# Performance work log

Hardware: AMD Instinct MI355X
Metric: run time of the kernel (lower is better)

The kernel has to match this reference:

```python
import jax, jax.numpy as jnp
import numpy as np

H_SZ, W_SZ = 24, 24  # size for location=2 (H*W == N3)

def _ln(x, g, b, eps=1e-5):
    m = jnp.mean(x, axis=-1, keepdims=True)
    v = jnp.var(x, axis=-1, keepdims=True)
    return (x - m) / jnp.sqrt(v + eps) * g + b

def _cross_attn(value, x2, Wp, bp):
    # key = softmax(x2^T, dim=1) == softmax over channels; query = softmax over tokens
    k = jax.nn.softmax(x2, axis=2)   # [B,M,C], softmax over C
    q = jax.nn.softmax(x2, axis=1)   # [B,M,C], softmax over M
    ctx = jnp.einsum('bnc,bmc->bnm', value, k)   # value @ key
    att = jnp.einsum('bnm,bmc->bnc', ctx, q)     # context @ query
    return att @ Wp.T + bp

def _dwconv(x, Wdw, bdw, Hh, Ww):
    B, N, C = x.shape
    t = x.transpose(0, 2, 1).reshape(B, C, Hh, Ww)
    y = jax.lax.conv_general_dilated(t, Wdw, (1, 1), 'SAME',
                                     feature_group_count=C,
                                     dimension_numbers=('NCHW', 'OIHW', 'NCHW'))
    y = y + bdw[None, :, None, None]
    return y.reshape(B, C, N).transpose(0, 2, 1)

def setup_inputs() -> dict:
    key = jax.random.key(0)
    ks = jax.random.split(key, 16)
    B = 4; d0, d1, d2 = 128, 256, 512
    N1, N2, N3 = 96 * 96, 48 * 48, 24 * 24
    s = 0.02
    dh = 4 * d2
    inp = {}
    inp['x']  = jax.random.normal(ks[0], (B, N1, d0), jnp.float32)
    inp['x2'] = jax.random.normal(ks[1], (B, N2, d1), jnp.float32)
    inp['x3'] = jax.random.normal(ks[2], (B, N3, d2), jnp.float32)
    inp['W_lin']  = jax.random.normal(ks[3], (d2, d0)) * s   # linear: d0->d2
    inp['W_lin2'] = jax.random.normal(ks[4], (d2, d1)) * s   # linear2: d1->d2
    inp['W_lin3'] = jax.random.normal(ks[5], (d1, d0)) * s   # linear3: d0->d1
    inp['W_lin4'] = jax.random.normal(ks[6], (d2, d1)) * s   # linear4: d1->d2
    inp['w'] = jnp.ones((1,), jnp.float32)
    inp['Wp1'] = jax.random.normal(ks[7], (d2, d2)) * s;  inp['bp1'] = jnp.zeros((d2,))
    inp['Wp2'] = jax.random.normal(ks[8], (d2, d2)) * s;  inp['bp2'] = jnp.zeros((d2,))
    inp['Wp3'] = jax.random.normal(ks[9], (d1, d1)) * s;  inp['bp3'] = jnp.zeros((d1,))
    inp['Wp4'] = jax.random.normal(ks[10], (d2, d2)) * s; inp['bp4'] = jnp.zeros((d2,))
    inp['g_norm'] = jnp.ones((d2,)); inp['b_norm'] = jnp.zeros((d2,))
    inp['Wfc1'] = jax.random.normal(ks[11], (dh, d2)) * s; inp['bfc1'] = jnp.zeros((dh,))
    inp['Wdw']  = jax.random.normal(ks[12], (dh, 1, 3, 3)) * s; inp['bdw'] = jnp.zeros((dh,))
    inp['g_ln1'] = jnp.ones((dh,)); inp['b_ln1'] = jnp.zeros((dh,))
    inp['Wfc2'] = jax.random.normal(ks[13], (d2, dh)) * s; inp['bfc2'] = jnp.zeros((d2,))
    return inp

def reference(x, x2, x3, W_lin, W_lin2, W_lin3, W_lin4, w,
              Wp1, bp1, Wp2, bp2, Wp3, bp3, Wp4, bp4,
              g_norm, b_norm, Wfc1, bfc1, Wdw, bdw, g_ln1, b_ln1, Wfc2, bfc2):
    # location == 2 branch
    image  = x  @ W_lin.T    # [B,N1,d2]
    image2 = x2 @ W_lin2.T   # [B,N2,d2]
    image4 = x  @ W_lin3.T   # [B,N1,d1]
    atten1 = _cross_attn(x3, image,  Wp1, bp1)
    atten2 = _cross_attn(x3, image2, Wp2, bp2)
    a3 = _cross_attn(x2, image4, Wp3, bp3)   # [B,N2,d1]
    a3 = a3 @ W_lin4.T                        # [B,N2,d2]
    atten3 = _cross_attn(x3, a3, Wp4, bp4)    # [B,N3,d2]
    f = jax.nn.sigmoid(w)
    other = (1.0 - f) / 2.0
    atten_ = f * atten3 + other * atten2 + other * atten1
    atten = x3 + atten_
    an = _ln(atten, g_norm, b_norm)
    # MixFFN_skip (fc1 computed once; torch computes it twice with same result)
    h = an @ Wfc1.T + bfc1
    dw = _dwconv(h, Wdw, bdw, H_SZ, W_SZ)
    ax = jax.nn.gelu(_ln(dw + h, g_ln1, b_ln1), approximate=False)
    out = ax @ Wfc2.T + bfc2
    return atten + out
```

## Files before the change

### kernel.cpp

```cpp
#include <hip/hip_runtime.h>
#include <hip/hip_bf16.h>
#include <math.h>

typedef long long i64;
typedef __attribute__((ext_vector_type(8))) short short8v;
typedef __attribute__((ext_vector_type(4))) float float4v;

#define SPITCH 72
#define NCV 13

__device__ __forceinline__ float ldv(const void* p, i64 idx, int isBf16) {
  return isBf16 ? __bfloat162float(((const __hip_bfloat16*)p)[idx])
                : ((const float*)p)[idx];
}
__device__ __forceinline__ unsigned short bf16bits(float f) {
  __hip_bfloat16 h = __float2bfloat16(f);
  return *(unsigned short*)&h;
}
__device__ __forceinline__ float bits2f(unsigned short u) {
  union { unsigned int ui; float fl; } cv; cv.ui = ((unsigned int)u) << 16;
  return cv.fl;
}

__global__ void detect_dtype(const unsigned short* w, int* dt) {
  dt[0] = (w[0] == 0) ? 0 : 1;
}

struct CvArgs {
  const void* src[NCV];
  unsigned short* dst[NCV];
  i64 n[NCV];
  int blkStart[NCV + 1];
};
__global__ __launch_bounds__(256) void convert_many(const int* dt, CvArgs a) {
  int au = dt[0];
  int bid = blockIdx.x;
  int lo = 0;
  #pragma unroll
  for (int i = 0; i < NCV; ++i) if (bid >= a.blkStart[i + 1]) lo = i + 1;
  const void* s = a.src[lo];
  unsigned short* d = a.dst[lo];
  i64 n = a.n[lo];
  i64 base = ((i64)(bid - a.blkStart[lo]) * 256 + threadIdx.x) * 4;
  if (base + 4 <= n) {
    #pragma unroll
    for (int j = 0; j < 4; ++j) d[base + j] = bf16bits(ldv(s, base + j, au));
  } else {
    for (; base < n; ++base) d[base] = bf16bits(ldv(s, base, au));
  }
}

__global__ void transpose_dw(const int* dt, const void* Wdw, unsigned short* Wdwt) {
  int au = dt[0];
  int i = blockIdx.x * 256 + threadIdx.x;
  if (i >= 9 * 2048) return;
  int k = i / 2048, ch = i % 2048;
  Wdwt[i] = bf16bits(ldv(Wdw, (i64)ch * 9 + k, au));
}

__global__ __launch_bounds__(256) void gemm_mfma_bt(
    const int* dt,
    const unsigned short* A, i64 bsA,
    const unsigned short* Bt, i64 bsB,
    const void* bias, int biasDt,
    const void* add, int addDt, i64 bsAdd,
    void* C, i64 bsC, int outMode,
    int M, int N, int K, int flags,
    const void* wPtr, int alphaMode,
    float* csP, float* rsP)
{
  __shared__ unsigned short Ash[64 * SPITCH];
  __shared__ unsigned short Bsh[64 * SPITCH];
  __shared__ unsigned short LT[64 * SPITCH];

  const int au = dt[0];
  const int bDt = (biasDt == 2) ? au : biasDt;
  const int aDt = (addDt == 2) ? au : addDt;

  const int b  = blockIdx.z;
  const int m0 = blockIdx.y * 64;
  const int n0 = blockIdx.x * 64;
  const int t = threadIdx.x;
  const int lane = t & 63, wave = t >> 6;
  const int wr = (wave >> 1) * 32, wc = (wave & 1) * 32;
  const int quad = lane >> 4, l15 = lane & 15;
  const unsigned short* Ab = A + (i64)b * bsA;
  const unsigned short* Bb = Bt + (i64)b * bsB;
  const int sr = t >> 3, sg = (t & 7) * 8;

  float alpha = 1.0f;
  if (alphaMode) {
    float w0 = ldv(wPtr, 0, au);
    float f = 1.0f / (1.0f + expf(-w0));
    alpha = (alphaMode == 2) ? f : (1.0f - f) * 0.5f;
  }

  float4v acc00 = {0.f,0.f,0.f,0.f}, acc01 = {0.f,0.f,0.f,0.f};
  float4v acc10 = {0.f,0.f,0.f,0.f}, acc11 = {0.f,0.f,0.f,0.f};

  for (int k0 = 0; k0 < K; k0 += 64) {
    #pragma unroll
    for (int p = 0; p < 2; ++p) {
      int rr = sr + p * 32;
      *(short8v*)&Ash[rr * SPITCH + sg] = *(const short8v*)&Ab[(i64)(m0 + rr) * K + k0 + sg];
      *(short8v*)&Bsh[rr * SPITCH + sg] = *(const short8v*)&Bb[(i64)(n0 + rr) * K + k0 + sg];
    }
    __syncthreads();
    #pragma unroll
    for (int ks = 0; ks < 2; ++ks) {
      int ko = ks * 32 + quad * 8;
      short8v a0 = *(const short8v*)&Ash[(wr + l15) * SPITCH + ko];
      short8v a1 = *(const short8v*)&Ash[(wr + 16 + l15) * SPITCH + ko];
      short8v b0 = *(const short8v*)&Bsh[(wc + l15) * SPITCH + ko];
      short8v b1 = *(const short8v*)&Bsh[(wc + 16 + l15) * SPITCH + ko];
      acc00 = __builtin_amdgcn_mfma_f32_16x16x32_bf16(a0, b0, acc00, 0, 0, 0);
      acc01 = __builtin_amdgcn_mfma_f32_16x16x32_bf16(a0, b1, acc01, 0, 0, 0);
      acc10 = __builtin_amdgcn_mfma_f32_16x16x32_bf16(a1, b0, acc10, 0, 0, 0);
      acc11 = __builtin_amdgcn_mfma_f32_16x16x32_bf16(a1, b1, acc11, 0, 0, 0);
    }
    __syncthreads();
  }

  float* Cf = (float*)C;
  unsigned short* Ch = (unsigned short*)C;

  if (outMode == 2) {
    #pragma unroll
    for (int rg = 0; rg < 4; ++rg) {
      #pragma unroll
      for (int sub = 0; sub < 4; ++sub) {
        int lr = wr + quad * 4 + rg + (sub >> 1) * 16;
        int lc = wc + l15 + (sub & 1) * 16;
        float v = (sub == 0 ? acc00[rg] : sub == 1 ? acc01[rg] :
                   sub == 2 ? acc10[rg] : acc11[rg]) * alpha;
        if (bias) v += ldv(bias, n0 + lc, bDt);
        if (flags & 1) v = expf(v);
        LT[lc * SPITCH + lr] = bf16bits(v);
      }
    }
    __syncthreads();
    #pragma unroll
    for (int p = 0; p < 2; ++p) {
      int rr = sr + p * 32;
      short8v vv = *(short8v*)&LT[rr * SPITCH + sg];
      *(short8v*)(Ch + (i64)b * bsC + (i64)(n0 + rr) * M + m0 + sg) = vv;
    }
    if (csP) {
      if (t < 64) {
        const unsigned short* Lr = &LT[t * SPITCH];
        float s = 0.f;
        #pragma unroll
        for (int i = 0; i < 64; ++i) s += bits2f(Lr[i]);
        atomicAdd(&csP[(i64)b * N + n0 + t], s);
      } else if (t < 128) {
        int tok = t - 64;
        float s = 0.f;
        #pragma unroll
        for (int i = 0; i < 64; ++i) s += bits2f(LT[i * SPITCH + tok]);
        atomicAdd(&rsP[(i64)b * M + m0 + tok], s);
      }
    }
    return;
  }

  #pragma unroll
  for (int rg = 0; rg < 4; ++rg) {
    #pragma unroll
    for (int sub = 0; sub < 4; ++sub) {
      int lr = wr + quad * 4 + rg + (sub >> 1) * 16;
      int lc = wc + l15 + (sub & 1) * 16;
      int gi = m0 + lr, gj = n0 + lc;
      float v = (sub == 0 ? acc00[rg] : sub == 1 ? acc01[rg] :
                 sub == 2 ? acc10[rg] : acc11[rg]) * alpha;
      if (bias) v += ldv(bias, gj, bDt);
      if (add)  v += ldv(add, (i64)b * bsAdd + (i64)gi * N + gj, aDt);
      i64 idx = (i64)b * bsC + (i64)gi * N + gj;
      if (flags & 2) v += Cf[idx];
      if (flags & 1) v = expf(v);
      if (outMode == 1) Ch[idx] = bf16bits(v);
      else              Cf[idx] = v;
    }
  }
}

__global__ __launch_bounds__(256) void softprod_sym(
    const unsigned short* Gt, const float* rs, float* Sraw,
    int C, i64 M, int splits, int mChunk)
{
  __shared__ unsigned short At[64 * SPITCH];
  __shared__ unsigned short Bt[64 * SPITCH];
  const int b  = blockIdx.z / splits;
  const int sp = blockIdx.z % splits;
  const int nStrips = C >> 6;
  int rem = blockIdx.x, s0 = 0;
  while (rem >= nStrips - s0) { rem -= nStrips - s0; ++s0; }
  const int s1 = s0 + rem;
  const int c0 = s0 * 64;
  const int c1 = s1 * 64;

  const int t = threadIdx.x;
  const int lane = t & 63, wave = t >> 6;
  const int wr = (wave >> 1) * 32, wc = (wave & 1) * 32;
  const int quad = lane >> 4, l15 = lane & 15;
  const unsigned short* Gb = Gt + (i64)b * C * M;
  const float* rib = rs + (i64)b * M;
  const int sr = t >> 3, sg = (t & 7) * 8;

  float4v acc00 = {0.f,0.f,0.f,0.f}, acc01 = {0.f,0.f,0.f,0.f};
  float4v acc10 = {0.f,0.f,0.f,0.f}, acc11 = {0.f,0.f,0.f,0.f};

  const i64 mBeg = (i64)sp * mChunk, mEnd = mBeg + mChunk;
  for (i64 m0 = mBeg; m0 < mEnd; m0 += 64) {
    float rv[8];
    #pragma unroll
    for (int j = 0; j < 8; ++j) rv[j] = rsqrtf(rib[m0 + sg + j]);
    #pragma unroll
    for (int p = 0; p < 2; ++p) {
      int rr = sr + p * 32;
      short8v va = *(const short8v*)&Gb[(i64)(c0 + rr) * M + m0 + sg];
      short8v vb = *(const short8v*)&Gb[(i64)(c1 + rr) * M + m0 + sg];
      short8v sa, sb;
      #pragma unroll
      for (int j = 0; j < 8; ++j) {
        sa[j] = (short)bf16bits(bits2f((unsigned short)va[j]) * rv[j]);
        sb[j] = (short)bf16bits(bits2f((unsigned short)vb[j]) * rv[j]);
      }
      *(short8v*)&At[rr * SPITCH + sg] = sa;
      *(short8v*)&Bt[rr * SPITCH + sg] = sb;
    }
    __syncthreads();
    #pragma unroll
    for (int ks = 0; ks < 2; ++ks) {
      int ko = ks * 32 + quad * 8;
      short8v a0 = *(const short8v*)&At[(wr + l15) * SPITCH + ko];
      short8v a1 = *(const short8v*)&At[(wr + 16 + l15) * SPITCH + ko];
      short8v b0 = *(const short8v*)&Bt[(wc + l15) * SPITCH + ko];
      short8v b1 = *(const short8v*)&Bt[(wc + 16 + l15) * SPITCH + ko];
      acc00 = __builtin_amdgcn_mfma_f32_16x16x32_bf16(a0, b0, acc00, 0, 0, 0);
      acc01 = __builtin_amdgcn_mfma_f32_16x16x32_bf16(a0, b1, acc01, 0, 0, 0);
      acc10 = __builtin_amdgcn_mfma_f32_16x16x32_bf16(a1, b0, acc10, 0, 0, 0);
      acc11 = __builtin_amdgcn_mfma_f32_16x16x32_bf16(a1, b1, acc11, 0, 0, 0);
    }
    __syncthreads();
  }

  float* Sb = Sraw + (i64)b * C * C;
  #pragma unroll
  for (int rg = 0; rg < 4; ++rg) {
    int r0 = c0 + wr + quad * 4 + rg;
    int cA = c1 + wc + l15;
    atomicAdd(&Sb[(i64)r0 * C + cA],             acc00[rg]);
    atomicAdd(&Sb[(i64)r0 * C + cA + 16],        acc01[rg]);
    atomicAdd(&Sb[(i64)(r0 + 16) * C + cA],      acc10[rg]);
    atomicAdd(&Sb[(i64)(r0 + 16) * C + cA + 16], acc11[rg]);
  }
}

__global__ __launch_bounds__(256) void softprod_sym128(
    const unsigned short* Gt, const float* rs, float* Sraw,
    int C, i64 M, int splits, int mChunk)
{
  __shared__ unsigned short Ash[128 * SPITCH];
  __shared__ unsigned short Bsh[128 * SPITCH];
  const int b  = blockIdx.z / splits;
  const int sp = blockIdx.z % splits;
  const int nStrips = C >> 7;
  int rem = blockIdx.x, s0 = 0;
  while (rem >= nStrips - s0) { rem -= nStrips - s0; ++s0; }
  const int s1 = s0 + rem;
  const int c0 = s0 * 128;
  const int c1 = s1 * 128;

  const int t = threadIdx.x;
  const int lane = t & 63, wave = t >> 6;
  const int wrow = (wave >> 1) * 64, wcol = (wave & 1) * 64;
  const int quad = lane >> 4, l15 = lane & 15;
  const unsigned short* Gb = Gt + (i64)b * C * M;
  const float* rib = rs + (i64)b * M;
  const int sg = (t & 7) * 8;

  float4v acc[4][4];
  #pragma unroll
  for (int i = 0; i < 4; ++i)
    #pragma unroll
    for (int j = 0; j < 4; ++j)
      acc[i][j] = (float4v){0.f, 0.f, 0.f, 0.f};

  const i64 mBeg = (i64)sp * mChunk, mEnd = mBeg + mChunk;
  for (i64 m0 = mBeg; m0 < mEnd; m0 += 64) {
    float rv[8];
    #pragma unroll
    for (int j = 0; j < 8; ++j) rv[j] = rsqrtf(rib[m0 + sg + j]);
    #pragma unroll
    for (int p = 0; p < 4; ++p) {
      int e = t + 256 * p;
      int row = e >> 3;
      short8v va = *(const short8v*)&Gb[(i64)(c0 + row) * M + m0 + sg];
      short8v vb = *(const short8v*)&Gb[(i64)(c1 + row) * M + m0 + sg];
      short8v sa, sb;
      #pragma unroll
      for (int j = 0; j < 8; ++j) {
        sa[j] = (short)bf16bits(bits2f((unsigned short)va[j]) * rv[j]);
        sb[j] = (short)bf16bits(bits2f((unsigned short)vb[j]) * rv[j]);
      }
      *(short8v*)&Ash[row * SPITCH + sg] = sa;
      *(short8v*)&Bsh[row * SPITCH + sg] = sb;
    }
    __syncthreads();
    #pragma unroll
    for (int ks = 0; ks < 2; ++ks) {
      int ko = ks * 32 + quad * 8;
      short8v af[4], bf[4];
      #pragma unroll
      for (int i = 0; i < 4; ++i) {
        af[i] = *(const short8v*)&Ash[(wrow + i * 16 + l15) * SPITCH + ko];
        bf[i] = *(const short8v*)&Bsh[(wcol + i * 16 + l15) * SPITCH + ko];
      }
      #pragma unroll
      for (int i = 0; i < 4; ++i)
        #pragma unroll
        for (int j = 0; j < 4; ++j)
          acc[i][j] = __builtin_amdgcn_mfma_f32_16x16x32_bf16(af[i], bf[j], acc[i][j], 0, 0, 0);
    }
    __syncthreads();
  }

  float* Sb = Sraw + (i64)b * C * C;
  #pragma unroll
  for (int i = 0; i < 4; ++i)
    #pragma unroll
    for (int rg = 0; rg < 4; ++rg) {
      int r = c0 + wrow + i * 16 + quad * 4 + rg;
      #pragma unroll
      for (int j = 0; j < 4; ++j) {
        int cc = c1 + wcol + j * 16 + l15;
        atomicAdd(&Sb[(i64)r * C + cc], acc[i][j][rg]);
      }
    }
}

__global__ void scale_S_sym_bf16(const float* Sraw, const float* cs,
                                 unsigned short* Sb, int C, i64 total) {
  i64 i = (i64)blockIdx.x * blockDim.x + threadIdx.x;
  if (i >= total) return;
  i64 cc2 = (i64)C * C;
  i64 b = i / cc2;
  i64 r = (i % cc2) / C;
  int cp = (int)(i % C);
  const float* Sb_ = Sraw + b * cc2;
  float v = (((int)r >> 6) <= (cp >> 6)) ? Sb_[r * C + cp] : Sb_[(i64)cp * C + r];
  Sb[i] = bf16bits(v / cs[b * C + cp]);
}

__global__ __launch_bounds__(256) void transpose_to_bf16(
    const float* T, unsigned short* Tt, int Nn) {
  __shared__ float tile[64][65];
  int b = blockIdx.z;
  int i0 = blockIdx.y * 64, j0 = blockIdx.x * 64;
  const float* Tb = T + (i64)b * Nn * Nn;
  unsigned short* Ttb = Tt + (i64)b * Nn * Nn;
  int t = threadIdx.x;
  int li = t >> 6, lj = t & 63;
  #pragma unroll
  for (int p = 0; p < 16; ++p)
    tile[li + p * 4][lj] = Tb[(i64)(i0 + li + p * 4) * Nn + j0 + lj];
  __syncthreads();
  #pragma unroll
  for (int p = 0; p < 16; ++p) {
    int row = li + p * 4;
    Ttb[(i64)(j0 + row) * Nn + i0 + lj] = bf16bits(tile[lj][row]);
  }
}

__global__ void combine_bias(const int* dt, const void* w, const void* bp1,
                             const void* bp2, const void* bp4, float* biasc) {
  int au = dt[0];
  int j = threadIdx.x;
  float w0 = ldv(w, 0, au);
  float f = 1.0f / (1.0f + expf(-w0));
  float other = (1.0f - f) * 0.5f;
  biasc[j] = f * ldv(bp4, j, au) + other * (ldv(bp1, j, au) + ldv(bp2, j, au));
}

__global__ __launch_bounds__(256) void layernorm512(const int* dt, const float* X,
                                                    const void* g, const void* be,
                                                    __hip_bfloat16* Y) {
  int au = dt[0];
  i64 row = blockIdx.x;
  const float* xr = X + row * 512;
  int t = threadIdx.x;
  float x0 = xr[t], x1 = xr[t + 256];
  float s = x0 + x1, q = x0 * x0 + x1 * x1;
  #pragma unroll
  for (int off = 32; off; off >>= 1) { s += __shfl_down(s, off); q += __shfl_down(q, off); }
  __shared__ float ws_[4], wq_[4];
  int lane = t & 63, wv = t >> 6;
  if (!lane) { ws_[wv] = s; wq_[wv] = q; }
  __syncthreads();
  float S = ws_[0] + ws_[1] + ws_[2] + ws_[3];
  float Q = wq_[0] + wq_[1] + wq_[2] + wq_[3];
  float mean = S * (1.f / 512.f);
  float var = Q * (1.f / 512.f) - mean * mean;
  float inv = rsqrtf(var + 1e-5f);
  Y[row * 512 + t]       = __float2bfloat16((x0 - mean) * inv * ldv(g, t, au) + ldv(be, t, au));
  Y[row * 512 + t + 256] = __float2bfloat16((x1 - mean) * inv * ldv(g, t + 256, au) + ldv(be, t + 256, au));
}

__global__ __launch_bounds__(256) void dwconv_ln_gelu(
    const int* dt,
    const unsigned short* h, const unsigned short* Wdwt, const void* bdw,
    const void* g, const void* be, unsigned short* ax)
{
  int au = dt[0];
  int n = blockIdx.x;
  int b = blockIdx.y;
  int y = n / 24, x = n % 24;
  const unsigned short* hb = h + (i64)b * 576 * 2048;
  int t = threadIdx.x;
  int ch0 = t * 8;

  float accv[8];
  #pragma unroll
  for (int j = 0; j < 8; ++j) accv[j] = ldv(bdw, ch0 + j, au);

  #pragma unroll
  for (int dy = 0; dy < 3; ++dy) {
    int yy = y + dy - 1;
    if (yy < 0 || yy >= 24) continue;
    #pragma unroll
    for (int dx = 0; dx < 3; ++dx) {
      int xx = x + dx - 1;
      if (xx < 0 || xx >= 24) continue;
      short8v hv = *(const short8v*)&hb[(i64)(yy * 24 + xx) * 2048 + ch0];
      short8v wv = *(const short8v*)&Wdwt[(i64)(dy * 3 + dx) * 2048 + ch0];
      #pragma unroll
      for (int j = 0; j < 8; ++j)
        accv[j] += bits2f((unsigned short)hv[j]) * bits2f((unsigned short)wv[j]);
    }
  }

  short8v hc = *(const short8v*)&hb[(i64)n * 2048 + ch0];
  float z[8];
  float s = 0.f, q = 0.f;
  #pragma unroll
  for (int j = 0; j < 8; ++j) {
    float zz = accv[j] + bits2f((unsigned short)hc[j]);
    z[j] = zz; s += zz; q += zz * zz;
  }

  #pragma unroll
  for (int off = 32; off; off >>= 1) { s += __shfl_down(s, off); q += __shfl_down(q, off); }
  __shared__ float ws_[4], wq_[4];
  int lane = t & 63, wv2 = t >> 6;
  if (!lane) { ws_[wv2] = s; wq_[wv2] = q; }
  __syncthreads();
  float S = ws_[0] + ws_[1] + ws_[2] + ws_[3];
  float Q = wq_[0] + wq_[1] + wq_[2] + wq_[3];
  float mean = S * (1.f / 2048.f);
  float var = Q * (1.f / 2048.f) - mean * mean;
  float inv = rsqrtf(var + 1e-5f);

  short8v ov;
  #pragma unroll
  for (int j = 0; j < 8; ++j) {
    float v = (z[j] - mean) * inv * ldv(g, ch0 + j, au) + ldv(be, ch0 + j, au);
    float gl = 0.5f * v * (1.0f + erff(v * 0.70710678118654752f));
    ov[j] = (short)bf16bits(gl);
  }
  *(short8v*)&ax[((i64)b * 576 + n) * 2048 + ch0] = ov;
}

extern "C" void kernel_launch(void* const* d_in, const int* in_sizes, int n_in,
                              void* d_out, int out_size, void* d_ws, size_t ws_size,
                              hipStream_t stream) {
  const int B = 4, N1 = 9216, N2 = 2304, N3 = 576;
  const int d0 = 128, d1 = 256, d2 = 512, dh = 2048;

  const void* x     = d_in[0];
  const void* x2    = d_in[1];
  const void* x3    = d_in[2];
  const void* Wlin  = d_in[3];
  const void* Wlin2 = d_in[4];
  const void* Wlin3 = d_in[5];
  const void* Wlin4 = d_in[6];
  const void* w     = d_in[7];
  const void* Wp1 = d_in[8];  const void* bp1 = d_in[9];
  const void* Wp2 = d_in[10]; const void* bp2 = d_in[11];
  const void* Wp3 = d_in[12]; const void* bp3 = d_in[13];
  const void* Wp4 = d_in[14]; const void* bp4 = d_in[15];
  const void* gnorm = d_in[16]; const void* bnorm = d_in[17];
  const void* Wfc1 = d_in[18]; const void* bfc1 = d_in[19];
  const void* Wdw  = d_in[20]; const void* bdw  = d_in[21];
  const void* gln1 = d_in[22]; const void* bln1 = d_in[23];
  const void* Wfc2 = d_in[24]; const void* bfc2 = d_in[25];

  char* base = (char*)d_ws;
  size_t o = 0;
  auto alloc = [&](size_t n) -> char* {
    char* r = base + o; o += (n + 255) & ~(size_t)255; return r;
  };

  int* dtFlag = (int*)alloc(256);
  char* arena = alloc((size_t)B * N1 * d2 * 2);
  float* rsBig   = (float*)alloc((size_t)B * N1 * 4);
  float* rsSmall = (float*)alloc((size_t)B * N2 * 4);
  size_t csBytes = (size_t)B * (d2 + d2 + d1 + d2) * 4;
  float* csAll = (float*)alloc(csBytes);
  float* cs1  = csAll;
  float* cs2  = cs1 + B * d2;
  float* cs4  = cs2 + B * d2;
  float* cs3b = cs4 + B * d1;
  float* Sraw  = (float*)alloc((size_t)B * d2 * d2 * 4);
  float* S3raw = (float*)alloc((size_t)B * d1 * d1 * 4);
  unsigned short* Sb16  = (unsigned short*)alloc((size_t)B * d2 * d2 * 2);
  unsigned short* S3b16 = (unsigned short*)alloc((size_t)B * d1 * d1 * 2);
  unsigned short* U3t   = (unsigned short*)alloc((size_t)B * d1 * d1 * 2);
  float* T     = (float*)alloc((size_t)B * d2 * d2 * 4);
  float* biasc = (float*)alloc((size_t)d2 * 4);
  unsigned short* xb  = (unsigned short*)alloc((size_t)B * N1 * d0 * 2);
  unsigned short* x2b = (unsigned short*)alloc((size_t)B * N2 * d1 * 2);
  unsigned short* x3b = (unsigned short*)alloc((size_t)B * N3 * d2 * 2);
  unsigned short* Wlinb  = (unsigned short*)alloc((size_t)d2 * d0 * 2);
  unsigned short* Wlin2b = (unsigned short*)alloc((size_t)d2 * d1 * 2);
  unsigned short* Wlin3b = (unsigned short*)alloc((size_t)d1 * d0 * 2);
  unsigned short* Wlin4b = (unsigned short*)alloc((size_t)d2 * d1 * 2);
  unsigned short* Wp1b = (unsigned short*)alloc((size_t)d2 * d2 * 2);
  unsigned short* Wp2b = (unsigned short*)alloc((size_t)d2 * d2 * 2);
  unsigned short* Wp3b = (unsigned short*)alloc((size_t)d1 * d1 * 2);
  unsigned short* Wp4b = (unsigned short*)alloc((size_t)d2 * d2 * 2);
  unsigned short* Wfc1b = (unsigned short*)alloc((size_t)dh * d2 * 2);
  unsigned short* Wfc2b = (unsigned short*)alloc((size_t)d2 * dh * 2);
  unsigned short* Wdwt  = (unsigned short*)alloc((size_t)9 * dh * 2);

  unsigned short* Et1    = (unsigned short*)arena;
  unsigned short* Et4    = (unsigned short*)arena;
  unsigned short* a3buf  = (unsigned short*)(arena + 18874368);
  unsigned short* EtA3b  = (unsigned short*)arena;
  unsigned short* Et2    = (unsigned short*)arena;
  float*          atten  = (float*)arena;
  __hip_bfloat16* an     = (__hip_bfloat16*)(arena + 4718592);
  unsigned short* hbuf   = (unsigned short*)(arena + 7077888);
  unsigned short* axb    = (unsigned short*)(arena + 16515072);
  unsigned short* Tt     = (unsigned short*)(arena + 28573696);

  detect_dtype<<<dim3(1), dim3(1), 0, stream>>>((const unsigned short*)w, dtFlag);
  hipMemsetAsync(csAll, 0, csBytes, stream);

  {
    CvArgs a;
    const void* srcs[NCV] = { x, x2, x3, Wlin, Wlin2, Wlin3, Wlin4,
                              Wp1, Wp2, Wp3, Wp4, Wfc1, Wfc2 };
    unsigned short* dsts[NCV] = { xb, x2b, x3b, Wlinb, Wlin2b, Wlin3b, Wlin4b,
                                  Wp1b, Wp2b, Wp3b, Wp4b, Wfc1b, Wfc2b };
    i64 ns[NCV] = { (i64)B*N1*d0, (i64)B*N2*d1, (i64)B*N3*d2,
                    (i64)d2*d0, (i64)d2*d1, (i64)d1*d0, (i64)d2*d1,
                    (i64)d2*d2, (i64)d2*d2, (i64)d1*d1, (i64)d2*d2,
                    (i64)dh*d2, (i64)d2*dh };
    int cum = 0;
    for (int i = 0; i < NCV; ++i) {
      a.src[i] = srcs[i]; a.dst[i] = dsts[i]; a.n[i] = ns[i];
      a.blkStart[i] = cum;
      cum += (int)((ns[i] + 1023) / 1024);
    }
    a.blkStart[NCV] = cum;
    convert_many<<<dim3(cum), dim3(256), 0, stream>>>(dtFlag, a);
    transpose_dw<<<dim3((9 * dh + 255) / 256), dim3(256), 0, stream>>>(dtFlag, Wdw, Wdwt);
  }

  auto gemm64 = [&](const unsigned short* A_, i64 bsA,
                    const unsigned short* Bt_, i64 bsB,
                    const void* bias_, int biasDt,
                    const void* add_, int addDt, i64 bsAdd,
                    void* C_, i64 bsC, int outMode,
                    int M_, int N_, int K_, int flags, int alphaMode,
                    float* csP = nullptr, float* rsP = nullptr) {
    gemm_mfma_bt<<<dim3(N_ / 64, M_ / 64, B), dim3(256), 0, stream>>>(
        dtFlag, A_, bsA, Bt_, bsB, bias_, biasDt, add_, addDt, bsAdd,
        C_, bsC, outMode, M_, N_, K_, flags, w, alphaMode, csP, rsP);
  };

  auto softtail = [&](unsigned short* Et, float* cs, float* rsArr,
                      float* SrawB, unsigned short* SbB, int C, int M, int splits,
                      bool use128) {
    hipMemsetAsync(SrawB, 0, (size_t)B * C * C * 4, stream);
    if (use128) {
      int nStrips = C / 128;
      int nPairs = nStrips * (nStrips + 1) / 2;
      softprod_sym128<<<dim3(nPairs, 1, B * splits), dim3(256), 0, stream>>>(
          Et, rsArr, SrawB, C, M, splits, M / splits);
    } else {
      int nStrips = C / 64;
      int nPairs = nStrips * (nStrips + 1) / 2;
      softprod_sym<<<dim3(nPairs, 1, B * splits), dim3(256), 0, stream>>>(
          Et, rsArr, SrawB, C, M, splits, M / splits);
    }
    i64 totS = (i64)B * C * C;
    scale_S_sym_bf16<<<dim3((unsigned)((totS + 255) / 256)), dim3(256), 0, stream>>>(
        SrawB, cs, SbB, C, totS);
  };

  hipMemsetAsync(rsBig, 0, (size_t)B * N1 * 4, stream);
  gemm64(xb, (i64)N1 * d0, Wlinb, 0, nullptr, 0, nullptr, 0, 0,
         Et1, (i64)N1 * d2, 2, N1, d2, d0, 1, 0, cs1, rsBig);
  softtail(Et1, cs1, rsBig, Sraw, Sb16, d2, N1, 12, true);
  gemm64(Sb16, (i64)d2 * d2, Wp1b, 0, nullptr, 0, nullptr, 0, 0,
         T, (i64)d2 * d2, 0, d2, d2, d2, 0, 1);

  hipMemsetAsync(rsBig, 0, (size_t)B * N1 * 4, stream);
  gemm64(xb, (i64)N1 * d0, Wlin3b, 0, nullptr, 0, nullptr, 0, 0,
         Et4, (i64)N1 * d1, 2, N1, d1, d0, 1, 0, cs4, rsBig);
  softtail(Et4, cs4, rsBig, S3raw, S3b16, d1, N1, 16, false);
  gemm64(S3b16, (i64)d1 * d1, Wp3b, 0, nullptr, 0, nullptr, 0, 0,
         U3t, (i64)d1 * d1, 2, d1, d1, d1, 0, 0);
  gemm64(x2b, (i64)N2 * d1, U3t, (i64)d1 * d1, bp3, 2, nullptr, 0, 0,
         a3buf, (i64)N2 * d1, 1, N2, d1, d1, 0, 0);
  hipMemsetAsync(rsSmall, 0, (size_t)B * N2 * 4, stream);
  gemm64(a3buf, (i64)N2 * d1, Wlin4b, 0, nullptr, 0, nullptr, 0, 0,
         EtA3b, (i64)N2 * d2, 2, N2, d2, d1, 1, 0, cs3b, rsSmall);
  softtail(EtA3b, cs3b, rsSmall, Sraw, Sb16, d2, N2, 6, true);
  gemm64(Sb16, (i64)d2 * d2, Wp4b, 0, nullptr, 0, nullptr, 0, 0,
         T, (i64)d2 * d2, 0, d2, d2, d2, 2, 2);

  hipMemsetAsync(rsSmall, 0, (size_t)B * N2 * 4, stream);
  gemm64(x2b, (i64)N2 * d1, Wlin2b, 0, nullptr, 0, nullptr, 0, 0,
         Et2, (i64)N2 * d2, 2, N2, d2, d1, 1, 0, cs2, rsSmall);
  softtail(Et2, cs2, rsSmall, Sraw, Sb16, d2, N2, 6, true);
  gemm64(Sb16, (i64)d2 * d2, Wp2b, 0, nullptr, 0, nullptr, 0, 0,
         T, (i64)d2 * d2, 0, d2, d2, d2, 2, 1);

  transpose_to_bf16<<<dim3(d2 / 64, d2 / 64, B), dim3(256), 0, stream>>>(T, Tt, d2);
  combine_bias<<<dim3(1), dim3(d2), 0, stream>>>(dtFlag, w, bp1, bp2, bp4, biasc);

  gemm64(x3b, (i64)N3 * d2, Tt, (i64)d2 * d2, biasc, 0, x3, 2, (i64)N3 * d2,
         atten, (i64)N3 * d2, 0, N3, d2, d2, 0, 0);

  layernorm512<<<dim3(B * N3), dim3(256), 0, stream>>>(dtFlag, atten, gnorm, bnorm, an);

  gemm64((const unsigned short*)an, (i64)N3 * d2, Wfc1b, 0, bfc1, 2, nullptr, 0, 0,
         hbuf, (i64)N3 * dh, 1, N3, dh, d2, 0, 0);

  dwconv_ln_gelu<<<dim3(N3, B), dim3(256), 0, stream>>>(
      dtFlag, hbuf, Wdwt, bdw, gln1, bln1, axb);

  gemm64(axb, (i64)N3 * dh, Wfc2b, 0, bfc2, 2,
         atten, 0, (i64)N3 * d2,
         d_out, (i64)N3 * d2, 0, N3, d2, dh, 0, 0);

  (void)in_sizes; (void)n_in; (void)out_size; (void)ws_size;
}
```

Before: 540.5 us.

## Double-buffer softmax-product kernel with register prefetch and unify on 128 tiles

```diff
diff --git a/kernel.cpp b/kernel.cpp
--- a/kernel.cpp
+++ b/kernel.cpp
@@ -183,85 +183,12 @@
   }
 }
 
-__global__ __launch_bounds__(256) void softprod_sym(
+__global__ __launch_bounds__(256, 2) void softprod128_db(
     const unsigned short* Gt, const float* rs, float* Sraw,
     int C, i64 M, int splits, int mChunk)
 {
-  __shared__ unsigned short At[64 * SPITCH];
-  __shared__ unsigned short Bt[64 * SPITCH];
-  const int b  = blockIdx.z / splits;
-  const int sp = blockIdx.z % splits;
-  const int nStrips = C >> 6;
-  int rem = blockIdx.x, s0 = 0;
-  while (rem >= nStrips - s0) { rem -= nStrips - s0; ++s0; }
-  const int s1 = s0 + rem;
-  const int c0 = s0 * 64;
-  const int c1 = s1 * 64;
-
-  const int t = threadIdx.x;
-  const int lane = t & 63, wave = t >> 6;
-  const int wr = (wave >> 1) * 32, wc = (wave & 1) * 32;
-  const int quad = lane >> 4, l15 = lane & 15;
-  const unsigned short* Gb = Gt + (i64)b * C * M;
-  const float* rib = rs + (i64)b * M;
-  const int sr = t >> 3, sg = (t & 7) * 8;
-
-  float4v acc00 = {0.f,0.f,0.f,0.f}, acc01 = {0.f,0.f,0.f,0.f};
-  float4v acc10 = {0.f,0.f,0.f,0.f}, acc11 = {0.f,0.f,0.f,0.f};
-
-  const i64 mBeg = (i64)sp * mChunk, mEnd = mBeg + mChunk;
-  for (i64 m0 = mBeg; m0 < mEnd; m0 += 64) {
-    float rv[8];
-    #pragma unroll
-    for (int j = 0; j < 8; ++j) rv[j] = rsqrtf(rib[m0 + sg + j]);
-    #pragma unroll
-    for (int p = 0; p < 2; ++p) {
-      int rr = sr + p * 32;
-      short8v va = *(const short8v*)&Gb[(i64)(c0 + rr) * M + m0 + sg];
-      short8v vb = *(const short8v*)&Gb[(i64)(c1 + rr) * M + m0 + sg];
-      short8v sa, sb;
-      #pragma unroll
-      for (int j = 0; j < 8; ++j) {
-        sa[j] = (short)bf16bits(bits2f((unsigned short)va[j]) * rv[j]);
-        sb[j] = (short)bf16bits(bits2f((unsigned short)vb[j]) * rv[j]);
-      }
-      *(short8v*)&At[rr * SPITCH + sg] = sa;
-      *(short8v*)&Bt[rr * SPITCH + sg] = sb;
-    }
-    __syncthreads();
-    #pragma unroll
-    for (int ks = 0; ks < 2; ++ks) {
-      int ko = ks * 32 + quad * 8;
-      short8v a0 = *(const short8v*)&At[(wr + l15) * SPITCH + ko];
-      short8v a1 = *(const short8v*)&At[(wr + 16 + l15) * SPITCH + ko];
-      short8v b0 = *(const short8v*)&Bt[(wc + l15) * SPITCH + ko];
-      short8v b1 = *(const short8v*)&Bt[(wc + 16 + l15) * SPITCH + ko];
-      acc00 = __builtin_amdgcn_mfma_f32_16x16x32_bf16(a0, b0, acc00, 0, 0, 0);
-      acc01 = __builtin_amdgcn_mfma_f32_16x16x32_bf16(a0, b1, acc01, 0, 0, 0);
-      acc10 = __builtin_amdgcn_mfma_f32_16x16x32_bf16(a1, b0, acc10, 0, 0, 0);
-      acc11 = __builtin_amdgcn_mfma_f32_16x16x32_bf16(a1, b1, acc11, 0, 0, 0);
-    }
-    __syncthreads();
-  }
-
-  float* Sb = Sraw + (i64)b * C * C;
-  #pragma unroll
-  for (int rg = 0; rg < 4; ++rg) {
-    int r0 = c0 + wr + quad * 4 + rg;
-    int cA = c1 + wc + l15;
-    atomicAdd(&Sb[(i64)r0 * C + cA],             acc00[rg]);
-    atomicAdd(&Sb[(i64)r0 * C + cA + 16],        acc01[rg]);
-    atomicAdd(&Sb[(i64)(r0 + 16) * C + cA],      acc10[rg]);
-    atomicAdd(&Sb[(i64)(r0 + 16) * C + cA + 16], acc11[rg]);
-  }
-}
-
-__global__ __launch_bounds__(256) void softprod_sym128(
-    const unsigned short* Gt, const float* rs, float* Sraw,
-    int C, i64 M, int splits, int mChunk)
-{
-  __shared__ unsigned short Ash[128 * SPITCH];
-  __shared__ unsigned short Bsh[128 * SPITCH];
+  __shared__ unsigned short Ash[2][128 * SPITCH];
+  __shared__ unsigned short Bsh[2][128 * SPITCH];
   const int b  = blockIdx.z / splits;
   const int sp = blockIdx.z % splits;
   const int nStrips = C >> 7;
@@ -278,6 +205,7 @@
   const unsigned short* Gb = Gt + (i64)b * C * M;
   const float* rib = rs + (i64)b * M;
   const int sg = (t & 7) * 8;
+  const int r4 = t >> 3;
 
   float4v acc[4][4];
   #pragma unroll
@@ -286,43 +214,69 @@
     for (int j = 0; j < 4; ++j)
       acc[i][j] = (float4v){0.f, 0.f, 0.f, 0.f};
 
-  const i64 mBeg = (i64)sp * mChunk, mEnd = mBeg + mChunk;
-  for (i64 m0 = mBeg; m0 < mEnd; m0 += 64) {
-    float rv[8];
-    #pragma unroll
-    for (int j = 0; j < 8; ++j) rv[j] = rsqrtf(rib[m0 + sg + j]);
+  const i64 mBeg = (i64)sp * mChunk;
+  const int nt = mChunk >> 6;
+
+  const unsigned short* Arow = &Gb[(i64)(c0 + r4) * M + sg];
+  const unsigned short* Brow = &Gb[(i64)(c1 + r4) * M + sg];
+
+  short8v pa[4], pb[4];
+  float rv[8];
+  {
+    i64 m0 = mBeg;
     #pragma unroll
     for (int p = 0; p < 4; ++p) {
-      int e = t + 256 * p;
-      int row = e >> 3;
-      short8v va = *(const short8v*)&Gb[(i64)(c0 + row) * M + m0 + sg];
-      short8v vb = *(const short8v*)&Gb[(i64)(c1 + row) * M + m0 + sg];
-      short8v sa, sb;
+      pa[p] = *(const short8v*)&Arow[(i64)32 * p * M + m0];
+      pb[p] = *(const short8v*)&Brow[(i64)32 * p * M + m0];
+    }
+    #pragma unroll
+    for (int j = 0; j < 8; ++j) {
+      float rr_ = rsqrtf(rib[m0 + sg + j]);
+      rv[j] = rr_ * rr_;
+    }
+  }
+
+  int cur = 0;
+  for (int tt = 0; tt < nt; ++tt) {
+    #pragma unroll
+    for (int p = 0; p < 4; ++p) {
+      *(short8v*)&Ash[cur][(r4 + 32 * p) * SPITCH + sg] = pa[p];
+      short8v sb;
+      #pragma unroll
+      for (int j = 0; j < 8; ++j)
+        sb[j] = (short)bf16bits(bits2f((unsigned short)pb[p][j]) * rv[j]);
+      *(short8v*)&Bsh[cur][(r4 + 32 * p) * SPITCH + sg] = sb;
+    }
+    __syncthreads();
+    if (tt + 1 < nt) {
+      i64 m0 = mBeg + (i64)(tt + 1) * 64;
+      #pragma unroll
+      for (int p = 0; p < 4; ++p) {
+        pa[p] = *(const short8v*)&Arow[(i64)32 * p * M + m0];
+        pb[p] = *(const short8v*)&Brow[(i64)32 * p * M + m0];
+      }
       #pragma unroll
       for (int j = 0; j < 8; ++j) {
-        sa[j] = (short)bf16bits(bits2f((unsigned short)va[j]) * rv[j]);
-        sb[j] = (short)bf16bits(bits2f((unsigned short)vb[j]) * rv[j]);
+        float rr_ = rsqrtf(rib[m0 + sg + j]);
+        rv[j] = rr_ * rr_;
       }
-      *(short8v*)&Ash[row * SPITCH + sg] = sa;
-      *(short8v*)&Bsh[row * SPITCH + sg] = sb;
-    }
-    __syncthreads();
+    }
     #pragma unroll
     for (int ks = 0; ks < 2; ++ks) {
       int ko = ks * 32 + quad * 8;
-      short8v af[4], bf[4];
+      short8v af[4], bfr[4];
       #pragma unroll
       for (int i = 0; i < 4; ++i) {
-        af[i] = *(const short8v*)&Ash[(wrow + i * 16 + l15) * SPITCH + ko];
-        bf[i] = *(const short8v*)&Bsh[(wcol + i * 16 + l15) * SPITCH + ko];
+        af[i]  = *(const short8v*)&Ash[cur][(wrow + i * 16 + l15) * SPITCH + ko];
+        bfr[i] = *(const short8v*)&Bsh[cur][(wcol + i * 16 + l15) * SPITCH + ko];
       }
       #pragma unroll
       for (int i = 0; i < 4; ++i)
         #pragma unroll
         for (int j = 0; j < 4; ++j)
-          acc[i][j] = __builtin_amdgcn_mfma_f32_16x16x32_bf16(af[i], bf[j], acc[i][j], 0, 0, 0);
-    }
-    __syncthreads();
+          acc[i][j] = __builtin_amdgcn_mfma_f32_16x16x32_bf16(af[i], bfr[j], acc[i][j], 0, 0, 0);
+    }
+    cur ^= 1;
   }
 
   float* Sb = Sraw + (i64)b * C * C;
@@ -580,20 +534,12 @@
   };
 
   auto softtail = [&](unsigned short* Et, float* cs, float* rsArr,
-                      float* SrawB, unsigned short* SbB, int C, int M, int splits,
-                      bool use128) {
+                      float* SrawB, unsigned short* SbB, int C, int M, int splits) {
     hipMemsetAsync(SrawB, 0, (size_t)B * C * C * 4, stream);
-    if (use128) {
-      int nStrips = C / 128;
-      int nPairs = nStrips * (nStrips + 1) / 2;
-      softprod_sym128<<<dim3(nPairs, 1, B * splits), dim3(256), 0, stream>>>(
-          Et, rsArr, SrawB, C, M, splits, M / splits);
-    } else {
-      int nStrips = C / 64;
-      int nPairs = nStrips * (nStrips + 1) / 2;
-      softprod_sym<<<dim3(nPairs, 1, B * splits), dim3(256), 0, stream>>>(
-          Et, rsArr, SrawB, C, M, splits, M / splits);
-    }
+    int nStrips = C / 128;
+    int nPairs = nStrips * (nStrips + 1) / 2;
+    softprod128_db<<<dim3(nPairs, 1, B * splits), dim3(256), 0, stream>>>(
+        Et, rsArr, SrawB, C, M, splits, M / splits);
     i64 totS = (i64)B * C * C;
     scale_S_sym_bf16<<<dim3((unsigned)((totS + 255) / 256)), dim3(256), 0, stream>>>(
         SrawB, cs, SbB, C, totS);
@@ -602,14 +548,14 @@
   hipMemsetAsync(rsBig, 0, (size_t)B * N1 * 4, stream);
   gemm64(xb, (i64)N1 * d0, Wlinb, 0, nullptr, 0, nullptr, 0, 0,
          Et1, (i64)N1 * d2, 2, N1, d2, d0, 1, 0, cs1, rsBig);
-  softtail(Et1, cs1, rsBig, Sraw, Sb16, d2, N1, 12, true);
+  softtail(Et1, cs1, rsBig, Sraw, Sb16, d2, N1, 12);
   gemm64(Sb16, (i64)d2 * d2, Wp1b, 0, nullptr, 0, nullptr, 0, 0,
          T, (i64)d2 * d2, 0, d2, d2, d2, 0, 1);
 
   hipMemsetAsync(rsBig, 0, (size_t)B * N1 * 4, stream);
   gemm64(xb, (i64)N1 * d0, Wlin3b, 0, nullptr, 0, nullptr, 0, 0,
          Et4, (i64)N1 * d1, 2, N1, d1, d0, 1, 0, cs4, rsBig);
-  softtail(Et4, cs4, rsBig, S3raw, S3b16, d1, N1, 16, false);
+  softtail(Et4, cs4, rsBig, S3raw, S3b16, d1, N1, 36);
   gemm64(S3b16, (i64)d1 * d1, Wp3b, 0, nullptr, 0, nullptr, 0, 0,
          U3t, (i64)d1 * d1, 2, d1, d1, d1, 0, 0);
   gemm64(x2b, (i64)N2 * d1, U3t, (i64)d1 * d1, bp3, 2, nullptr, 0, 0,
@@ -617,14 +563,14 @@
   hipMemsetAsync(rsSmall, 0, (size_t)B * N2 * 4, stream);
   gemm64(a3buf, (i64)N2 * d1, Wlin4b, 0, nullptr, 0, nullptr, 0, 0,
          EtA3b, (i64)N2 * d2, 2, N2, d2, d1, 1, 0, cs3b, rsSmall);
-  softtail(EtA3b, cs3b, rsSmall, Sraw, Sb16, d2, N2, 6, true);
+  softtail(EtA3b, cs3b, rsSmall, Sraw, Sb16, d2, N2, 12);
   gemm64(Sb16, (i64)d2 * d2, Wp4b, 0, nullptr, 0, nullptr, 0, 0,
          T, (i64)d2 * d2, 0, d2, d2, d2, 2, 2);
 
   hipMemsetAsync(rsSmall, 0, (size_t)B * N2 * 4, stream);
   gemm64(x2b, (i64)N2 * d1, Wlin2b, 0, nullptr, 0, nullptr, 0, 0,
          Et2, (i64)N2 * d2, 2, N2, d2, d1, 1, 0, cs2, rsSmall);
-  softtail(Et2, cs2, rsSmall, Sraw, Sb16, d2, N2, 6, true);
+  softtail(Et2, cs2, rsSmall, Sraw, Sb16, d2, N2, 12);
   gemm64(Sb16, (i64)d2 * d2, Wp2b, 0, nullptr, 0, nullptr, 0, 0,
          T, (i64)d2 * d2, 0, d2, d2, d2, 2, 1);
 
```

New measurement: 562.1 us. +4.0%, slower.
